# Kernel optimization log

Hardware: AMD Instinct MI355X
Metric: run time of the kernel (lower is better)

Reference implementation:

```python
import jax, jax.numpy as jnp
import numpy as np

HEADS = 8
DIM_HEAD = 64


def setup_inputs() -> dict:
    key = jax.random.key(0)
    ks = jax.random.split(key, 10)
    B, NQ, NK, D, INNER = 4, 2048, 2048, 1024, HEADS * DIM_HEAD
    w_scale = 0.02
    return {
        "x": jax.random.normal(ks[0], (B, NQ, D), jnp.float32),
        "context": jax.random.normal(ks[1], (B, NK, D), jnp.float32),
        "wq": jax.random.normal(ks[2], (D, INNER), jnp.float32) * w_scale,
        "bq": jax.random.normal(ks[3], (INNER,), jnp.float32) * w_scale,
        "wk": jax.random.normal(ks[4], (D, INNER), jnp.float32) * w_scale,
        "bk": jax.random.normal(ks[5], (INNER,), jnp.float32) * w_scale,
        "wv": jax.random.normal(ks[6], (D, INNER), jnp.float32) * w_scale,
        "bv": jax.random.normal(ks[7], (INNER,), jnp.float32) * w_scale,
        "wo": jax.random.normal(ks[8], (INNER, D), jnp.float32) * w_scale,
        "bo": jax.random.normal(ks[9], (D,), jnp.float32) * w_scale,
    }


def _split_heads(t):
    # [b, n, h*d] -> [b, h, n, d]
    b, n, _ = t.shape
    return t.reshape(b, n, HEADS, DIM_HEAD).transpose(0, 2, 1, 3)


def reference(x, context, wq, bq, wk, bk, wv, bv, wo, bo):
    scale = DIM_HEAD ** -0.5
    q = _split_heads(x @ wq + bq)        # [b, h, nq, d]
    k = _split_heads(context @ wk + bk)  # [b, h, nk, d]
    v = _split_heads(context @ wv + bv)  # [b, h, nk, d]
    sim = jnp.einsum('bhid,bhjd->bhij', q, k) * scale  # full score matrix, as in original
    attn = jax.nn.softmax(sim, axis=-1)
    out = jnp.einsum('bhij,bhjd->bhid', attn, v)       # [b, h, nq, d]
    b, h, n, d = out.shape
    out = out.transpose(0, 2, 1, 3).reshape(b, n, h * d)
    return out @ wo + bo
```

## Files before the change

kernel.cpp:

```cpp
#include <hip/hip_runtime.h>
#include <hip/hip_bf16.h>

typedef __attribute__((ext_vector_type(8))) short short8;
typedef __attribute__((ext_vector_type(4))) float f32x4;
typedef __attribute__((ext_vector_type(2))) unsigned uint2u;

__device__ __forceinline__ short f2bf(float f) {
  union { float f; unsigned u; } x; x.f = f;
  unsigned r = x.u + 0x7fffu + ((x.u >> 16) & 1u);
  return (short)(r >> 16);
}

__device__ __forceinline__ void gload16(const short* g, short* l) {
  __builtin_amdgcn_global_load_lds(
      (const __attribute__((address_space(1))) unsigned*)g,
      (__attribute__((address_space(3))) unsigned*)l, 16, 0, 0);
}

__global__ void cast2_bf16_kernel(const float* __restrict__ a,
                                  const float* __restrict__ b,
                                  short* __restrict__ dst) {
  int i = (blockIdx.x * 256 + threadIdx.x) * 4;
  const float* s = (i < (1 << 23)) ? a : b;
  int j = i & ((1 << 23) - 1);
  float4 f = *(const float4*)(s + j);
  union { short s[4]; uint2 u; } o;
  o.s[0] = f2bf(f.x); o.s[1] = f2bf(f.y);
  o.s[2] = f2bf(f.z); o.s[3] = f2bf(f.w);
  *(uint2*)(dst + i) = o.u;
}

__global__ __launch_bounds__(256) void transpose_cast4_kernel(
    const float* __restrict__ wq, const float* __restrict__ wk,
    const float* __restrict__ wv, const float* __restrict__ wo,
    short* __restrict__ wqt, short* __restrict__ wkt,
    short* __restrict__ wvt, short* __restrict__ wot) {
  __shared__ short tile[64][72];
  int z = blockIdx.z;
  const float* src = (z == 0) ? wq : (z == 1) ? wk : (z == 2) ? wv : wo;
  short* dst = (z == 0) ? wqt : (z == 1) ? wkt : (z == 2) ? wvt : wot;
  int R = (z < 3) ? 1024 : 512, C = (z < 3) ? 512 : 1024;
  int tpc = C >> 6;
  int bx = blockIdx.x % tpc, by = blockIdx.x / tpc;
  int r0 = by * 64, c0 = bx * 64;
  int tx = threadIdx.x & 15, ty = threadIdx.x >> 4;
#pragma unroll
  for (int i = 0; i < 4; i++) {
    int r = i * 16 + ty;
    float4 f = *(const float4*)(src + (size_t)(r0 + r) * C + c0 + tx * 4);
    union { short s[4]; uint2 u; } o;
    o.s[0] = f2bf(f.x); o.s[1] = f2bf(f.y);
    o.s[2] = f2bf(f.z); o.s[3] = f2bf(f.w);
    *(uint2*)&tile[r][tx * 4] = o.u;
  }
  __syncthreads();
#pragma unroll
  for (int i = 0; i < 4; i++) {
    int c = i * 16 + ty;
    union { short s[4]; uint2 u; } o;
#pragma unroll
    for (int k = 0; k < 4; k++) o.s[k] = tile[tx * 4 + k][c];
    *(uint2*)(dst + (size_t)(c0 + c) * R + r0 + tx * 4) = o.u;
  }
}

__device__ __forceinline__ void gemm_core(
    const short* __restrict__ A, const short* __restrict__ Bt, int K,
    int mblk, int nblk, short* sA, short* sB, f32x4 (&acc)[4][4]) {
  int tid = threadIdx.x;
  int lane = tid & 63, wave = tid >> 6;
  int quad = lane >> 4, l15 = lane & 15;
  int wm = (wave >> 1) * 64, wn = (wave & 1) * 64;
  int sub = lane >> 3, e8 = lane & 7;
  int swz = (e8 ^ sub) << 3;
  int s0 = (quad ^ (l15 & 7)) << 3;
  const short* Ag = A + (size_t)(mblk + 32 * wave + sub) * K + swz;
  const short* Bg = Bt + (size_t)(nblk + 32 * wave + sub) * K + swz;
  short* Al = sA + 4 * wave * 512;
  short* Bl = sB + 4 * wave * 512;

  for (int k0 = 0; k0 < K; k0 += 64) {
    __syncthreads();
#pragma unroll
    for (int t = 0; t < 4; t++) {
      gload16(Ag + (size_t)(8 * t) * K + k0, Al + t * 512);
      gload16(Bg + (size_t)(8 * t) * K + k0, Bl + t * 512);
    }
    __syncthreads();
#pragma unroll
    for (int h = 0; h < 2; h++) {
      int so = s0 ^ (h << 5);
      short8 af[4], bf[4];
#pragma unroll
      for (int mt = 0; mt < 4; mt++)
        af[mt] = *(const short8*)(&sA[(wm + mt * 16 + l15) * 64 + so]);
#pragma unroll
      for (int nt = 0; nt < 4; nt++)
        bf[nt] = *(const short8*)(&sB[(wn + nt * 16 + l15) * 64 + so]);
#pragma unroll
      for (int mt = 0; mt < 4; mt++)
#pragma unroll
        for (int nt = 0; nt < 4; nt++)
          acc[mt][nt] = __builtin_amdgcn_mfma_f32_16x16x32_bf16(
              af[mt], bf[nt], acc[mt][nt], 0, 0, 0);
    }
  }
}

__global__ __launch_bounds__(256) void gemm_qkv(
    const short* __restrict__ xb, const short* __restrict__ cb,
    const short* __restrict__ wqt, const short* __restrict__ wkt,
    const short* __restrict__ wvt,
    const float* __restrict__ bq, const float* __restrict__ bk,
    const float* __restrict__ bv,
    short* __restrict__ Qb, short* __restrict__ Kb, short* __restrict__ Vt) {
  __shared__ __align__(16) short sA[128 * 64];
  __shared__ __align__(16) short sB[128 * 64];
  int z = blockIdx.z;
  const short* A  = (z == 0) ? xb : cb;
  const short* Bt = (z == 0) ? wqt : (z == 1) ? wkt : wvt;
  const float* bias = (z == 0) ? bq : (z == 1) ? bk : bv;
  short* out = (z == 0) ? Qb : (z == 1) ? Kb : Vt;
  float scale = (z == 0) ? 0.18033688011112042f : 1.0f;
  int mblk = blockIdx.x * 128, nblk = blockIdx.y * 128;
  f32x4 acc[4][4] = {};
  gemm_core(A, Bt, 1024, mblk, nblk, sA, sB, acc);

  int lane = threadIdx.x & 63, wave = threadIdx.x >> 6;
  int quad = lane >> 4, l15 = lane & 15;
  int wm = (wave >> 1) * 64, wn = (wave & 1) * 64;
#pragma unroll
  for (int nt = 0; nt < 4; nt++) {
    int col = nblk + wn + nt * 16 + l15;
    float bias_v = bias[col];
    int h = col >> 6, dh = col & 63;
#pragma unroll
    for (int mt = 0; mt < 4; mt++)
#pragma unroll
      for (int r = 0; r < 4; r++) {
        int row = mblk + wm + mt * 16 + quad * 4 + r;
        float v = (acc[mt][nt][r] + bias_v) * scale;
        int b = row >> 11, n = row & 2047;
        size_t base = ((size_t)(b * 8 + h)) << 17;
        size_t idx = (z == 2) ? base + ((size_t)dh << 11) + n
                              : base + ((size_t)n << 6) + dh;
        out[idx] = f2bf(v);
      }
  }
}

__global__ __launch_bounds__(256) void gemm_out(
    const short* __restrict__ Ob, const short* __restrict__ wot,
    const float* __restrict__ bo, float* __restrict__ out) {
  __shared__ __align__(16) short sA[128 * 64];
  __shared__ __align__(16) short sB[128 * 64];
  int mblk = blockIdx.x * 128, nblk = blockIdx.y * 128;
  f32x4 acc[4][4] = {};
  gemm_core(Ob, wot, 512, mblk, nblk, sA, sB, acc);
  int lane = threadIdx.x & 63, wave = threadIdx.x >> 6;
  int quad = lane >> 4, l15 = lane & 15;
  int wm = (wave >> 1) * 64, wn = (wave & 1) * 64;
#pragma unroll
  for (int nt = 0; nt < 4; nt++) {
    int col = nblk + wn + nt * 16 + l15;
    float bias_v = bo[col];
#pragma unroll
    for (int mt = 0; mt < 4; mt++)
#pragma unroll
      for (int r = 0; r < 4; r++) {
        int row = mblk + wm + mt * 16 + quad * 4 + r;
        out[(size_t)row * 1024 + col] = acc[mt][nt][r] + bias_v;
      }
  }
}

__global__ __launch_bounds__(256, 2) void attn_kernel(
    const short* __restrict__ Qb, const short* __restrict__ Kb,
    const short* __restrict__ Vt, short* __restrict__ Ob) {
  __shared__ __align__(16) short sK[2 * 64 * 64];
  __shared__ __align__(16) short sV[2 * 64 * 64];
  int tid = threadIdx.x;
  int lane = tid & 63, wave = tid >> 6;
  int quad = lane >> 4, l15 = lane & 15;
  int bh = blockIdx.x & 31, qt = blockIdx.x >> 5;
  const short* Qp = Qb + ((size_t)bh << 17);
  const short* Kp = Kb + ((size_t)bh << 17);
  const short* Vp = Vt + ((size_t)bh << 17);
  int qrow0 = qt * 128 + wave * 32;

  short8 qf[2][2];
#pragma unroll
  for (int g = 0; g < 2; g++) {
    const short* qrow = Qp + (size_t)(qrow0 + g * 16 + l15) * 64;
    qf[g][0] = *(const short8*)(qrow + quad * 8);
    qf[g][1] = *(const short8*)(qrow + 32 + quad * 8);
  }

  int jk0 = 2 * wave, jk1 = 2 * wave + 1;
  int sub = lane >> 3;
  int e8  = lane & 7;
  int swz = (e8 ^ sub) << 3;
  const short* kg0 = Kp + (size_t)(8 * jk0 + sub) * 64 + e8 * 8;
  const short* kg1 = Kp + (size_t)(8 * jk1 + sub) * 64 + e8 * 8;
  const short* vg0 = Vp + (size_t)(8 * jk0 + sub) * 2048 + e8 * 8;
  const short* vg1 = Vp + (size_t)(8 * jk1 + sub) * 2048 + e8 * 8;
  int kw0 = (8 * jk0 + sub) * 64 + swz;
  int kw1 = (8 * jk1 + sub) * 64 + swz;

  int s0 = (quad ^ (l15 & 7)) << 3;
  int s1 = s0 ^ 32;

  f32x4 o[2][4] = {};
  float lsum[2] = {0.f, 0.f};

  uint4 rk0 = *(const uint4*)kg0, rk1 = *(const uint4*)kg1;
  uint4 rv0 = *(const uint4*)vg0, rv1 = *(const uint4*)vg1;
  *(uint4*)(sK + kw0) = rk0; *(uint4*)(sK + kw1) = rk1;
  *(uint4*)(sV + kw0) = rv0; *(uint4*)(sV + kw1) = rv1;
  rk0 = *(const uint4*)(kg0 + 4096); rk1 = *(const uint4*)(kg1 + 4096);
  rv0 = *(const uint4*)(vg0 + 64);   rv1 = *(const uint4*)(vg1 + 64);
  __syncthreads();

  for (int it = 0; it < 32; ++it) {
    const short* sKr = sK + (it & 1) * 4096;
    const short* sVr = sV + (it & 1) * 4096;
    if (it < 31) {
      short* sKw = sK + ((it & 1) ^ 1) * 4096;
      short* sVw = sV + ((it & 1) ^ 1) * 4096;
      *(uint4*)(sKw + kw0) = rk0; *(uint4*)(sKw + kw1) = rk1;
      *(uint4*)(sVw + kw0) = rv0; *(uint4*)(sVw + kw1) = rv1;
      if (it < 30) {
        size_t ko = (size_t)(it + 2) * 4096, vo = (size_t)(it + 2) * 64;
        rk0 = *(const uint4*)(kg0 + ko); rk1 = *(const uint4*)(kg1 + ko);
        rv0 = *(const uint4*)(vg0 + vo); rv1 = *(const uint4*)(vg1 + vo);
      }
    }
    unsigned xp[2][4][2];
#pragma unroll
    for (int jt = 0; jt < 4; jt++) {
      short8 k0 = *(const short8*)(&sKr[(jt * 16 + l15) * 64 + s0]);
      short8 k1 = *(const short8*)(&sKr[(jt * 16 + l15) * 64 + s1]);
#pragma unroll
      for (int g = 0; g < 2; g++) {
        f32x4 zz = {0.f, 0.f, 0.f, 0.f};
        zz = __builtin_amdgcn_mfma_f32_16x16x32_bf16(k0, qf[g][0], zz, 0, 0, 0);
        f32x4 st = __builtin_amdgcn_mfma_f32_16x16x32_bf16(k1, qf[g][1], zz, 0, 0, 0);
        float p0 = exp2f(st[0]), p1 = exp2f(st[1]);
        float p2 = exp2f(st[2]), p3 = exp2f(st[3]);
        lsum[g] += (p0 + p1) + (p2 + p3);
        union { __hip_bfloat162 b; unsigned u; } a0, a1;
        a0.b = __float22bfloat162_rn(make_float2(p0, p1));
        a1.b = __float22bfloat162_rn(make_float2(p2, p3));
        xp[g][jt][0] = a0.u; xp[g][jt][1] = a1.u;
      }
    }
    short8 pf[2][2];
#pragma unroll
    for (int g = 0; g < 2; g++) {
#pragma unroll
      for (int hb = 0; hb < 2; hb++) {
        unsigned x0 = xp[g][2 * hb][0], x1 = xp[g][2 * hb][1];
        unsigned x2 = xp[g][2 * hb + 1][0], x3 = xp[g][2 * hb + 1][1];
        uint2u r1 = __builtin_amdgcn_permlane32_swap(x0, x2, false, false);
        uint2u r2 = __builtin_amdgcn_permlane16_swap(r1[0], r1[1], false, false);
        uint2u r3 = __builtin_amdgcn_permlane32_swap(x1, x3, false, false);
        uint2u r4 = __builtin_amdgcn_permlane16_swap(r3[0], r3[1], false, false);
        union { unsigned u[4]; short8 s; } P;
        P.u[0] = r2[0]; P.u[1] = r4[0]; P.u[2] = r2[1]; P.u[3] = r4[1];
        pf[g][hb] = P.s;
      }
    }
#pragma unroll
    for (int nt = 0; nt < 4; nt++) {
      short8 v0 = *(const short8*)(&sVr[(nt * 16 + l15) * 64 + s0]);
      short8 v1 = *(const short8*)(&sVr[(nt * 16 + l15) * 64 + s1]);
#pragma unroll
      for (int g = 0; g < 2; g++) {
        o[g][nt] = __builtin_amdgcn_mfma_f32_16x16x32_bf16(v0, pf[g][0], o[g][nt], 0, 0, 0);
        o[g][nt] = __builtin_amdgcn_mfma_f32_16x16x32_bf16(v1, pf[g][1], o[g][nt], 0, 0, 0);
      }
    }
    if (it < 31) __syncthreads();
  }

  int b = bh >> 3, h = bh & 7;
#pragma unroll
  for (int g = 0; g < 2; g++) {
    float l = lsum[g];
    l += __shfl_xor(l, 16, 64);
    l += __shfl_xor(l, 32, 64);
    float inv = 1.0f / l;
    size_t rowbase = ((size_t)b * 2048 + qrow0 + g * 16 + l15) * 512 + h * 64 + quad * 4;
#pragma unroll
    for (int nt = 0; nt < 4; nt++) {
      union { short s[4]; uint2 u; } pk2;
#pragma unroll
      for (int r = 0; r < 4; r++) pk2.s[r] = f2bf(o[g][nt][r] * inv);
      *(uint2*)(Ob + rowbase + nt * 16) = pk2.u;
    }
  }
}

extern "C" void kernel_launch(void* const* d_in, const int* in_sizes, int n_in,
                              void* d_out, int out_size, void* d_ws, size_t ws_size,
                              hipStream_t stream) {
  const float* x   = (const float*)d_in[0];
  const float* ctx = (const float*)d_in[1];
  const float* wq  = (const float*)d_in[2];
  const float* bq  = (const float*)d_in[3];
  const float* wk  = (const float*)d_in[4];
  const float* bk  = (const float*)d_in[5];
  const float* wv  = (const float*)d_in[6];
  const float* bv  = (const float*)d_in[7];
  const float* wo  = (const float*)d_in[8];
  const float* bo  = (const float*)d_in[9];
  float* out = (float*)d_out;
  char* ws = (char*)d_ws;

  short* xb  = (short*)(ws);
  short* cb  = (short*)(ws + (16ull << 20));
  short* wqt = (short*)(ws + (32ull << 20));
  short* wkt = (short*)(ws + (33ull << 20));
  short* wvt = (short*)(ws + (34ull << 20));
  short* wot = (short*)(ws + (35ull << 20));
  short* Qb  = (short*)(ws + (36ull << 20));
  short* Kb  = (short*)(ws + (44ull << 20));
  short* Vt  = (short*)(ws + (52ull << 20));
  short* Ob  = (short*)(ws + (60ull << 20));

  cast2_bf16_kernel<<<16384, 256, 0, stream>>>(x, ctx, xb);
  transpose_cast4_kernel<<<dim3(128, 1, 4), 256, 0, stream>>>(
      wq, wk, wv, wo, wqt, wkt, wvt, wot);
  gemm_qkv<<<dim3(64, 4, 3), 256, 0, stream>>>(xb, cb, wqt, wkt, wvt,
                                               bq, bk, bv, Qb, Kb, Vt);
  attn_kernel<<<512, 256, 0, stream>>>(Qb, Kb, Vt, Ob);
  gemm_out<<<dim3(64, 8), 256, 0, stream>>>(Ob, wot, bo, out);
}
```

Before: 248.0 us.

## Split attention over two KV halves and merge partials in a combine kernel

Each attention block now handles half of the key/value sequence, which doubles the grid to 1024 blocks and raises the launch-bounds occupancy hint to 4 blocks per CU. Blocks write unnormalized fp32 output partials and row sums into workspace regions that are free by then. A new combine kernel adds the two partials, normalizes them and casts the result to bf16 for the output GEMM. The aim is more parallelism and better latency hiding in attention. The cost is an extra launch, about 32MB of fp32 partials written and read back, and possible register pressure under the tighter occupancy bound.

New measurement: 251.4 us. Within noise of the previous version (+1.4%).

```diff
diff --git a/kernel.cpp b/kernel.cpp
--- a/kernel.cpp
+++ b/kernel.cpp
@@ -174,19 +174,23 @@
   }
 }
 
-__global__ __launch_bounds__(256, 2) void attn_kernel(
+__global__ __launch_bounds__(256, 4) void attn_kernel(
     const short* __restrict__ Qb, const short* __restrict__ Kb,
-    const short* __restrict__ Vt, short* __restrict__ Ob) {
+    const short* __restrict__ Vt, float* __restrict__ Op,
+    float* __restrict__ Ls) {
   __shared__ __align__(16) short sK[2 * 64 * 64];
   __shared__ __align__(16) short sV[2 * 64 * 64];
   int tid = threadIdx.x;
   int lane = tid & 63, wave = tid >> 6;
   int quad = lane >> 4, l15 = lane & 15;
-  int bh = blockIdx.x & 31, qt = blockIdx.x >> 5;
+  int bh = blockIdx.x & 31;
+  int qt = (blockIdx.x >> 5) & 15;
+  int ks = blockIdx.x >> 9;
   const short* Qp = Qb + ((size_t)bh << 17);
   const short* Kp = Kb + ((size_t)bh << 17);
   const short* Vp = Vt + ((size_t)bh << 17);
   int qrow0 = qt * 128 + wave * 32;
+  int t0 = ks * 16;
 
   short8 qf[2][2];
 #pragma unroll
@@ -213,24 +217,29 @@
   f32x4 o[2][4] = {};
   float lsum[2] = {0.f, 0.f};
 
-  uint4 rk0 = *(const uint4*)kg0, rk1 = *(const uint4*)kg1;
-  uint4 rv0 = *(const uint4*)vg0, rv1 = *(const uint4*)vg1;
+  uint4 rk0 = *(const uint4*)(kg0 + (size_t)t0 * 4096);
+  uint4 rk1 = *(const uint4*)(kg1 + (size_t)t0 * 4096);
+  uint4 rv0 = *(const uint4*)(vg0 + (size_t)t0 * 64);
+  uint4 rv1 = *(const uint4*)(vg1 + (size_t)t0 * 64);
   *(uint4*)(sK + kw0) = rk0; *(uint4*)(sK + kw1) = rk1;
   *(uint4*)(sV + kw0) = rv0; *(uint4*)(sV + kw1) = rv1;
-  rk0 = *(const uint4*)(kg0 + 4096); rk1 = *(const uint4*)(kg1 + 4096);
-  rv0 = *(const uint4*)(vg0 + 64);   rv1 = *(const uint4*)(vg1 + 64);
+  rk0 = *(const uint4*)(kg0 + (size_t)(t0 + 1) * 4096);
+  rk1 = *(const uint4*)(kg1 + (size_t)(t0 + 1) * 4096);
+  rv0 = *(const uint4*)(vg0 + (size_t)(t0 + 1) * 64);
+  rv1 = *(const uint4*)(vg1 + (size_t)(t0 + 1) * 64);
   __syncthreads();
 
-  for (int it = 0; it < 32; ++it) {
+  for (int it = 0; it < 16; ++it) {
     const short* sKr = sK + (it & 1) * 4096;
     const short* sVr = sV + (it & 1) * 4096;
-    if (it < 31) {
+    if (it < 15) {
       short* sKw = sK + ((it & 1) ^ 1) * 4096;
       short* sVw = sV + ((it & 1) ^ 1) * 4096;
       *(uint4*)(sKw + kw0) = rk0; *(uint4*)(sKw + kw1) = rk1;
       *(uint4*)(sVw + kw0) = rv0; *(uint4*)(sVw + kw1) = rv1;
-      if (it < 30) {
-        size_t ko = (size_t)(it + 2) * 4096, vo = (size_t)(it + 2) * 64;
+      if (it < 14) {
+        size_t ko = (size_t)(t0 + it + 2) * 4096;
+        size_t vo = (size_t)(t0 + it + 2) * 64;
         rk0 = *(const uint4*)(kg0 + ko); rk1 = *(const uint4*)(kg1 + ko);
         rv0 = *(const uint4*)(vg0 + vo); rv1 = *(const uint4*)(vg1 + vo);
       }
@@ -280,25 +289,47 @@
         o[g][nt] = __builtin_amdgcn_mfma_f32_16x16x32_bf16(v1, pf[g][1], o[g][nt], 0, 0, 0);
       }
     }
-    if (it < 31) __syncthreads();
+    if (it < 15) __syncthreads();
   }
 
   int b = bh >> 3, h = bh & 7;
+  float* Opb = Op + ((size_t)ks << 22);
 #pragma unroll
   for (int g = 0; g < 2; g++) {
     float l = lsum[g];
     l += __shfl_xor(l, 16, 64);
     l += __shfl_xor(l, 32, 64);
-    float inv = 1.0f / l;
+    if (lane < 16)
+      Ls[(ks << 16) + (bh << 11) + qrow0 + g * 16 + lane] = l;
     size_t rowbase = ((size_t)b * 2048 + qrow0 + g * 16 + l15) * 512 + h * 64 + quad * 4;
 #pragma unroll
-    for (int nt = 0; nt < 4; nt++) {
-      union { short s[4]; uint2 u; } pk2;
-#pragma unroll
-      for (int r = 0; r < 4; r++) pk2.s[r] = f2bf(o[g][nt][r] * inv);
-      *(uint2*)(Ob + rowbase + nt * 16) = pk2.u;
-    }
-  }
+    for (int nt = 0; nt < 4; nt++)
+      *(f32x4*)(Opb + rowbase + nt * 16) = o[g][nt];
+  }
+}
+
+__global__ __launch_bounds__(256) void combine_kernel(
+    const float* __restrict__ Op, const float* __restrict__ Ls,
+    short* __restrict__ Ob) {
+  int i = (blockIdx.x * 256 + threadIdx.x) * 8;
+  int row = i >> 9, colb = i & 511;
+  int b = row >> 11, n = row & 2047, h = colb >> 6;
+  int lsi = (((b << 3) + h) << 11) + n;
+  float inv = 1.0f / (Ls[lsi] + Ls[65536 + lsi]);
+  const float* p0 = Op + i;
+  const float* p1 = Op + (1u << 22) + i;
+  float4 a0 = *(const float4*)p0, a1 = *(const float4*)(p0 + 4);
+  float4 b0 = *(const float4*)p1, b1 = *(const float4*)(p1 + 4);
+  union { short s[8]; uint4 u; } o;
+  o.s[0] = f2bf((a0.x + b0.x) * inv);
+  o.s[1] = f2bf((a0.y + b0.y) * inv);
+  o.s[2] = f2bf((a0.z + b0.z) * inv);
+  o.s[3] = f2bf((a0.w + b0.w) * inv);
+  o.s[4] = f2bf((a1.x + b1.x) * inv);
+  o.s[5] = f2bf((a1.y + b1.y) * inv);
+  o.s[6] = f2bf((a1.z + b1.z) * inv);
+  o.s[7] = f2bf((a1.w + b1.w) * inv);
+  *(uint4*)(Ob + i) = o.u;
 }
 
 extern "C" void kernel_launch(void* const* d_in, const int* in_sizes, int n_in,
@@ -327,12 +358,15 @@
   short* Kb  = (short*)(ws + (44ull << 20));
   short* Vt  = (short*)(ws + (52ull << 20));
   short* Ob  = (short*)(ws + (60ull << 20));
+  float* Op  = (float*)(ws);
+  float* Ls  = (float*)(ws + (32ull << 20));
 
   cast2_bf16_kernel<<<16384, 256, 0, stream>>>(x, ctx, xb);
   transpose_cast4_kernel<<<dim3(128, 1, 4), 256, 0, stream>>>(
       wq, wk, wv, wo, wqt, wkt, wvt, wot);
   gemm_qkv<<<dim3(64, 4, 3), 256, 0, stream>>>(xb, cb, wqt, wkt, wvt,
                                                bq, bk, bv, Qb, Kb, Vt);
-  attn_kernel<<<512, 256, 0, stream>>>(Qb, Kb, Vt, Ob);
+  attn_kernel<<<1024, 256, 0, stream>>>(Qb, Kb, Vt, Op, Ls);
+  combine_kernel<<<2048, 256, 0, stream>>>(Op, Ls, Ob);
   gemm_out<<<dim3(64, 8), 256, 0, stream>>>(Ob, wot, bo, out);
 }
```
